# Performance work log

Hardware: AMD Instinct MI355X
Metric: run time of the kernel (lower is better)

Reference implementation:

```python
import jax, jax.numpy as jnp
import numpy as np

N_NODES = 50000


def gcn_conv(x, W, b, row, col, n):
    """PyG GCNConv with default add_self_loops=True, normalize=True.
    out[i] = sum_{e: col[e]=i} d^-1/2[row[e]] d^-1/2[i] * (x@W)[row[e]]
             + d^-1[i]*(x@W)[i] + b,  where d = in-degree + 1 (self-loop).
    """
    x_lin = x @ W                                   # [n, out_ch]
    ones = jnp.ones(row.shape[0], dtype=x.dtype)
    deg = jax.ops.segment_sum(ones, col, num_segments=n) + 1.0  # self-loop
    dinv = jax.lax.rsqrt(deg)                       # deg >= 1, safe
    norm = dinv[row] * dinv[col]                    # [E]
    msg = norm[:, None] * x_lin[row]                # [E, out_ch]
    agg = jax.ops.segment_sum(msg, col, num_segments=n)
    self_term = (dinv * dinv)[:, None] * x_lin      # self-loop contribution
    return agg + self_term + b


def setup_inputs() -> dict:
    key = jax.random.key(0)
    ks = jax.random.split(key, 10)
    in_ch, hid, out_ch = 128, 256, 64
    E = 800000
    x = jax.random.normal(ks[0], (N_NODES, in_ch), dtype=jnp.float32)
    edge_attr = jax.random.normal(ks[1], (E, 8), dtype=jnp.float32)  # unused by forward
    edge_index = jax.random.randint(ks[2], (2, E), 0, N_NODES, dtype=jnp.int64)
    def glorot(k, fan_in, fan_out):
        s = float(np.sqrt(6.0 / (fan_in + fan_out)))
        return jax.random.uniform(k, (fan_in, fan_out), jnp.float32, -s, s)
    return {
        "x": x,
        "edge_attr": edge_attr,
        "edge_index": edge_index,
        "W1": glorot(ks[3], in_ch, hid), "b1": jnp.zeros((hid,), jnp.float32),
        "W2": glorot(ks[4], hid, hid),  "b2": jnp.zeros((hid,), jnp.float32),
        "W3": glorot(ks[5], hid, out_ch), "b3": jnp.zeros((out_ch,), jnp.float32),
    }


def reference(x, edge_attr, edge_index, W1, b1, W2, b2, W3, b3):
    n = x.shape[0]
    row, col = edge_index[0], edge_index[1]
    h = jax.nn.sigmoid(gcn_conv(x, W1, b1, row, col, n))
    h = jax.nn.sigmoid(gcn_conv(h, W2, b2, row, col, n))
    # dropout(p=0.1) in eval mode is identity
    return gcn_conv(h, W3, b3, row, col, n)
```

## Files before the change

kernel.cpp:

```cpp
#include <hip/hip_runtime.h>
#include <hip/hip_bf16.h>

typedef __bf16 bf16x8_t __attribute__((ext_vector_type(8)));
typedef float f32x4_t __attribute__((ext_vector_type(4)));
typedef float f32x2_t __attribute__((ext_vector_type(2)));

__device__ __forceinline__ float bits2f(unsigned int u) {
    union { unsigned int u; float f; } c; c.u = u; return c.f;
}
__device__ __forceinline__ unsigned short f2bf_bits(float f) {
    __hip_bfloat16 h = __float2bfloat16(f);
    return __builtin_bit_cast(unsigned short, h);
}
__device__ __forceinline__ f32x2_t unpack_bf2(unsigned int u) {
    return (f32x2_t){bits2f(u << 16), bits2f(u & 0xffff0000u)};
}
__device__ __forceinline__ f32x2_t xsw(f32x2_t v, int off) {
    f32x2_t r;
    r[0] = __shfl_xor(v[0], off);
    r[1] = __shfl_xor(v[1], off);
    return r;
}

__global__ void sentinel_fill(float* __restrict__ out, int n) {
    int i = blockIdx.x * blockDim.x + threadIdx.x;
    if (i < n) out[i] = 100.0f;
}

__global__ void detect_ei(const unsigned int* __restrict__ ei, int* __restrict__ flags) {
    int lane = threadIdx.x;
    int cz = 0;
    #pragma unroll
    for (int j = 0; j < 4; ++j) {
        int idx = lane * 4 + j;
        cz += (ei[2 * idx + 1] == 0u);
    }
    #pragma unroll
    for (int off = 32; off; off >>= 1) cz += __shfl_down(cz, off);
    if (lane == 0) flags[0] = (cz > 200);
}


__global__ void count_rank_dual2(const int* __restrict__ ei, int* __restrict__ cnt,
                                 int* __restrict__ rank, int* __restrict__ c32,
                                 int* __restrict__ r32, int E, int M,
                                 const int* __restrict__ flags) {
    int e = blockIdx.x * blockDim.x + threadIdx.x;
    if (e < E) {
        int r, c;
        if (flags[0]) { r = ei[2 * e]; c = ei[2 * E + 2 * e]; }
        else          { r = ei[e];     c = ei[E + e]; }
        c32[e] = c;
        r32[e] = r;
        int rk = 0;
        if ((unsigned)c < (unsigned)M) rk = atomicAdd(&cnt[c], 1);
        rank[e] = rk;
    }
}

__global__ void scan_blocks(const int* __restrict__ cnt, int* __restrict__ excl,
                            int* __restrict__ bsum, int n) {
    int tid = threadIdx.x;
    int i = blockIdx.x * 256 + tid;
    int lane = tid & 63, wv = tid >> 6;
    __shared__ int ws[4];
    int v = (i < n) ? cnt[i] : 0;
    int s = v;
    #pragma unroll
    for (int off = 1; off < 64; off <<= 1) {
        int t = __shfl_up(s, off);
        if (lane >= off) s += t;
    }
    if (lane == 63) ws[wv] = s;
    __syncthreads();
    if (tid == 0) { int a = 0; for (int q = 0; q < 4; ++q) { int t = ws[q]; ws[q] = a; a += t; } }
    __syncthreads();
    int ex = s - v + ws[wv];
    if (i < n) excl[i] = ex;
    if (tid == 255) bsum[blockIdx.x] = ex + v;
}

__global__ void scan_bsums(const int* __restrict__ bsum, int* __restrict__ boff,
                           int nb, int* __restrict__ colptr, int n) {
    int tid = threadIdx.x, lane = tid & 63, wv = tid >> 6;
    __shared__ int ws[4];
    __shared__ int carry;
    if (tid == 0) carry = 0;
    __syncthreads();
    for (int base = 0; base < nb; base += 256) {
        int i = base + tid;
        int v = (i < nb) ? bsum[i] : 0;
        int s = v;
        #pragma unroll
        for (int off = 1; off < 64; off <<= 1) {
            int t = __shfl_up(s, off);
            if (lane >= off) s += t;
        }
        if (lane == 63) ws[wv] = s;
        __syncthreads();
        if (tid == 0) { int a = carry; for (int q = 0; q < 4; ++q) { int t = ws[q]; ws[q] = a; a += t; } carry = a; }
        __syncthreads();
        int ex = s - v + ws[wv];
        if (i < nb) boff[i] = ex;
        __syncthreads();
    }
    if (tid == 0) colptr[n] = carry;
}

__global__ void scan_add_dinv(const int* __restrict__ excl, const int* __restrict__ boff,
                              const int* __restrict__ cnt, int* __restrict__ colptr,
                              float* __restrict__ dinv, int n) {
    int i = blockIdx.x * 256 + threadIdx.x;
    if (i < n) {
        colptr[i] = excl[i] + boff[blockIdx.x];
        dinv[i] = rsqrtf((float)cnt[i] + 1.0f);
    }
}

__global__ void fill_csr_part2(const int* __restrict__ c32, const int* __restrict__ r32,
                               const int* __restrict__ colptr, const int* __restrict__ rank,
                               int* __restrict__ esrc, int E, int M, int psz) {
    int part = blockIdx.x & 7;
    int e = (blockIdx.x >> 3) * 256 + threadIdx.x;
    int lo = part * psz;
    int hi = lo + psz; if (hi > M) hi = M;
    if (e < E) {
        int c = c32[e];
        if (c >= lo && c < hi) {
            int r = r32[e];
            if ((unsigned)r < (unsigned)M) {
                int p = colptr[c] + rank[e];
                if ((unsigned)p < (unsigned)E) esrc[p] = r;
            }
        }
    }
}

__global__ void transpose_all(const float* __restrict__ W1, const float* __restrict__ W2,
                              const float* __restrict__ W3,
                              unsigned short* __restrict__ Wt1, unsigned short* __restrict__ Wt2,
                              unsigned short* __restrict__ Wt3) {
    int i = blockIdx.x * 256 + threadIdx.x;
    if (i < 32768) {
        int k = i >> 8, n = i & 255;
        Wt1[n * 128 + k] = f2bf_bits(W1[i]);
    } else if (i < 32768 + 65536) {
        int j = i - 32768;
        int k = j >> 8, n = j & 255;
        Wt2[n * 256 + k] = f2bf_bits(W2[j]);
    } else if (i < 114688) {
        int j = i - 98304;
        int k = j >> 6, n = j & 63;
        Wt3[n * 256 + k] = f2bf_bits(W3[j]);
    }
}

__global__ void prescale_x(const float* __restrict__ x, const float* __restrict__ dinv,
                           unsigned short* __restrict__ xs, int M, int total) {
    int i = blockIdx.x * 256 + threadIdx.x;
    if (i < total) {
        int row = i >> 7;
        int k = i & 127;
        xs[(size_t)(k >> 6) * ((size_t)M * 64) + (size_t)row * 64 + (k & 63)] =
            f2bf_bits(x[i] * dinv[row]);
    }
}

template<int K, int BN, int NTOT, int EPI>
__global__ __launch_bounds__(256) void gemm_tile(
    const __bf16* __restrict__ A,
    const unsigned short* __restrict__ Bt,
    const float* __restrict__ dinv,
    const float* __restrict__ bias,
    void* __restrict__ Y,
    int M)
{
    constexpr int KS = (K > 128) ? 128 : K;
    constexpr int KP = KS + 8;
    constexpr int NT = BN / 2 / 16;
    __shared__ unsigned short Bs[BN * KP];

    const int tid  = threadIdx.x;
    const int lane = tid & 63;
    const int wave = tid >> 6;
    const int wm   = wave >> 1;
    const int wn   = wave & 1;
    const int quad = lane >> 4;
    const int l16  = lane & 15;
    const int n0   = blockIdx.y * BN;

    int mrow[4];
#pragma unroll
    for (int mt = 0; mt < 4; ++mt) {
        int r = blockIdx.x * 128 + wm * 64 + mt * 16 + l16;
        mrow[mt] = (r < M) ? r : (M - 1);
    }

    f32x4_t acc[4][NT];
#pragma unroll
    for (int mt = 0; mt < 4; ++mt)
#pragma unroll
        for (int t = 0; t < NT; ++t) acc[mt][t] = (f32x4_t){0.f, 0.f, 0.f, 0.f};

    const unsigned short* BsW = &Bs[(wn * (BN / 2)) * KP];

    for (int kh = 0; kh < K; kh += KS) {
        constexpr int CH = BN * KS / 8;
        for (int idx = tid; idx < CH; idx += 256) {
            int n  = idx / (KS / 8);
            int k8 = idx - n * (KS / 8);
            uint4 v = *(const uint4*)(Bt + (size_t)(n0 + n) * K + kh + k8 * 8);
            *(uint4*)&Bs[n * KP + k8 * 8] = v;
        }
        __syncthreads();

#pragma unroll
        for (int kc = 0; kc < KS; kc += 32) {
            bf16x8_t a[4], b[NT];
#pragma unroll
            for (int mt = 0; mt < 4; ++mt)
                a[mt] = *(const bf16x8_t*)(A + (size_t)mrow[mt] * K + kh + kc + quad * 8);
#pragma unroll
            for (int t = 0; t < NT; ++t)
                b[t] = *(const bf16x8_t*)&BsW[(t * 16 + l16) * KP + kc + quad * 8];
#pragma unroll
            for (int mt = 0; mt < 4; ++mt)
#pragma unroll
                for (int t = 0; t < NT; ++t)
                    acc[mt][t] = __builtin_amdgcn_mfma_f32_16x16x32_bf16(a[mt], b[t], acc[mt][t], 0, 0, 0);
        }
        if (kh + KS < K) __syncthreads();
    }

    float bv[NT];
    if constexpr (EPI == 1) {
#pragma unroll
        for (int t = 0; t < NT; ++t)
            bv[t] = bias[n0 + wn * (BN / 2) + t * 16 + l16];
    }

#pragma unroll
    for (int mt = 0; mt < 4; ++mt) {
        int rowbase = blockIdx.x * 128 + wm * 64 + mt * 16 + quad * 4;
#pragma unroll
        for (int r = 0; r < 4; ++r) {
            int rrow = rowbase + r;
            if (rrow < M) {
                if constexpr (EPI == 0) {
                    float dv = dinv[rrow];
#pragma unroll
                    for (int t = 0; t < NT; ++t) {
                        int ccol = n0 + wn * (BN / 2) + t * 16 + l16;
                        ((__hip_bfloat16*)Y)[(size_t)rrow * NTOT + ccol] =
                            __float2bfloat16(acc[mt][t][r] * dv);
                    }
                } else if constexpr (EPI == 1) {
#pragma unroll
                    for (int t = 0; t < NT; ++t) {
                        int ccol = n0 + wn * (BN / 2) + t * 16 + l16;
                        float o = acc[mt][t][r] + bv[t];
                        o = 1.f / (1.f + __expf(-o));
                        ((__hip_bfloat16*)Y)[(size_t)rrow * NTOT + ccol] = __float2bfloat16(o);
                    }
                } else {
                    float dv = dinv[rrow];
#pragma unroll
                    for (int t = 0; t < NT; ++t) {
                        int ccol = n0 + wn * (BN / 2) + t * 16 + l16;
                        float o = acc[mt][t][r] * dv;
                        int pk = __builtin_amdgcn_cvt_pk_fp8_f32(o, o, 0, false);
                        size_t choff = (size_t)(ccol >> 7) * ((size_t)M * 128)
                                     + (size_t)rrow * 128 + (ccol & 127);
                        ((unsigned char*)Y)[choff] = (unsigned char)(pk & 0xff);
                    }
                }
            }
        }
    }
}

__global__ __launch_bounds__(256) void aggregate_fp8_c2(
    const unsigned char* __restrict__ Y8c,
    const int* __restrict__ colptr,
    const int* __restrict__ esrc,
    const float* __restrict__ dinv,
    const float* __restrict__ bias,
    unsigned short* __restrict__ H,
    int M, int Etot, int nbx)
{
    const int lane = threadIdx.x & 63;
    const int wave = threadIdx.x >> 6;
    const int sub = lane & 15;
    const int grp = lane >> 4;
    int bx = blockIdx.x;
    int chunk = (bx >= nbx) ? 1 : 0;
    if (chunk) bx -= nbx;
    int node = bx * 4 + wave;
    if (node >= M) return;

    int s = colptr[node];
    int e = colptr[node + 1];
    if (s < 0) s = 0;
    if (e > Etot) e = Etot;
    if (e < s) e = s;
    int n = e - s;

    const char* Yb = (const char*)(Y8c + (size_t)chunk * ((size_t)M * 128));
    const unsigned lb = (unsigned)(sub * 8);

    f32x2_t a0 = {0.f, 0.f}, a1 = {0.f, 0.f}, a2 = {0.f, 0.f}, a3 = {0.f, 0.f};

    if (grp == 0) {
        uint2 u = *(const uint2*)(Yb + ((unsigned)node) * 128u + lb);
        a0 += __builtin_amdgcn_cvt_pk_f32_fp8(u.x, false);
        a1 += __builtin_amdgcn_cvt_pk_f32_fp8(u.x, true);
        a2 += __builtin_amdgcn_cvt_pk_f32_fp8(u.y, false);
        a3 += __builtin_amdgcn_cvt_pk_f32_fp8(u.y, true);
    }
#pragma unroll 2
    for (int t = grp; t < n; t += 4) {
        unsigned off = ((unsigned)esrc[s + t]) * 128u + lb;
        uint2 u = *(const uint2*)(Yb + off);
        a0 += __builtin_amdgcn_cvt_pk_f32_fp8(u.x, false);
        a1 += __builtin_amdgcn_cvt_pk_f32_fp8(u.x, true);
        a2 += __builtin_amdgcn_cvt_pk_f32_fp8(u.y, false);
        a3 += __builtin_amdgcn_cvt_pk_f32_fp8(u.y, true);
    }

    a0 += xsw(a0, 16); a1 += xsw(a1, 16); a2 += xsw(a2, 16); a3 += xsw(a3, 16);
    a0 += xsw(a0, 32); a1 += xsw(a1, 32); a2 += xsw(a2, 32); a3 += xsw(a3, 32);

    if (grp == 0) {
        float dv = dinv[node];
        int chb = chunk * 128 + sub * 8;
        float4 b0 = *(const float4*)(bias + chb);
        float4 b1 = *(const float4*)(bias + chb + 4);
        float o[8];
        o[0] = a0[0] * dv + b0.x; o[1] = a0[1] * dv + b0.y;
        o[2] = a1[0] * dv + b0.z; o[3] = a1[1] * dv + b0.w;
        o[4] = a2[0] * dv + b1.x; o[5] = a2[1] * dv + b1.y;
        o[6] = a3[0] * dv + b1.z; o[7] = a3[1] * dv + b1.w;
        #pragma unroll
        for (int k = 0; k < 8; ++k) o[k] = 1.f / (1.f + __expf(-o[k]));
        uint4 st;
        st.x = (unsigned)f2bf_bits(o[0]) | ((unsigned)f2bf_bits(o[1]) << 16);
        st.y = (unsigned)f2bf_bits(o[2]) | ((unsigned)f2bf_bits(o[3]) << 16);
        st.z = (unsigned)f2bf_bits(o[4]) | ((unsigned)f2bf_bits(o[5]) << 16);
        st.w = (unsigned)f2bf_bits(o[6]) | ((unsigned)f2bf_bits(o[7]) << 16);
        *(uint4*)(H + (size_t)node * 256 + chb) = st;
    }
}

__global__ __launch_bounds__(256) void aggregate_bf16_c2(
    const unsigned short* __restrict__ Xc,
    const int* __restrict__ colptr,
    const int* __restrict__ esrc,
    const float* __restrict__ dinv,
    unsigned short* __restrict__ Hout,
    int M, int Etot, int nbx)
{
    const int lane = threadIdx.x & 63;
    const int wave = threadIdx.x >> 6;
    const int sub = lane & 15;
    const int grp = lane >> 4;
    int bx = blockIdx.x;
    int chunk = (bx >= nbx) ? 1 : 0;
    if (chunk) bx -= nbx;
    int node = bx * 4 + wave;
    if (node >= M) return;

    int s = colptr[node];
    int e = colptr[node + 1];
    if (s < 0) s = 0;
    if (e > Etot) e = Etot;
    if (e < s) e = s;
    int n = e - s;

    const char* Yb = (const char*)(Xc + (size_t)chunk * ((size_t)M * 64));
    const unsigned lb = (unsigned)(sub * 8);

    f32x2_t a0 = {0.f, 0.f}, a1 = {0.f, 0.f};

    if (grp == 0) {
        uint2 u = *(const uint2*)(Yb + ((unsigned)node) * 128u + lb);
        a0 += unpack_bf2(u.x);
        a1 += unpack_bf2(u.y);
    }
#pragma unroll 2
    for (int t = grp; t < n; t += 4) {
        unsigned off = ((unsigned)esrc[s + t]) * 128u + lb;
        uint2 u = *(const uint2*)(Yb + off);
        a0 += unpack_bf2(u.x);
        a1 += unpack_bf2(u.y);
    }

    a0 += xsw(a0, 16); a1 += xsw(a1, 16);
    a0 += xsw(a0, 32); a1 += xsw(a1, 32);

    if (grp == 0) {
        float dv = dinv[node];
        uint2 st;
        st.x = (unsigned)f2bf_bits(a0[0] * dv) | ((unsigned)f2bf_bits(a0[1] * dv) << 16);
        st.y = (unsigned)f2bf_bits(a1[0] * dv) | ((unsigned)f2bf_bits(a1[1] * dv) << 16);
        *(uint2*)(Hout + (size_t)node * 128 + chunk * 64 + sub * 4) = st;
    }
}

__global__ __launch_bounds__(256) void aggregate_bf16_64_v3(
    const unsigned short* __restrict__ Yin,
    const int* __restrict__ colptr,
    const int* __restrict__ esrc,
    const float* __restrict__ dinv,
    const float* __restrict__ bias,
    float* __restrict__ out,
    int M, int Etot)
{
    const int lane = threadIdx.x & 63;
    const int wave = threadIdx.x >> 6;
    const int sub = lane & 15;
    const int grp = lane >> 4;
    int node = blockIdx.x * 4 + wave;
    if (node >= M) return;

    int s = colptr[node];
    int e = colptr[node + 1];
    if (s < 0) s = 0;
    if (e > Etot) e = Etot;
    if (e < s) e = s;
    int n = e - s;

    const char* Yb = (const char*)Yin;
    const unsigned lb = (unsigned)(sub * 8);

    f32x2_t a0 = {0.f, 0.f}, a1 = {0.f, 0.f};

    if (grp == 0) {
        uint2 u = *(const uint2*)(Yb + ((unsigned)node) * 128u + lb);
        a0 += unpack_bf2(u.x);
        a1 += unpack_bf2(u.y);
    }
#pragma unroll 2
    for (int t = grp; t < n; t += 4) {
        unsigned off = ((unsigned)esrc[s + t]) * 128u + lb;
        uint2 u = *(const uint2*)(Yb + off);
        a0 += unpack_bf2(u.x);
        a1 += unpack_bf2(u.y);
    }

    a0 += xsw(a0, 16); a1 += xsw(a1, 16);
    a0 += xsw(a0, 32); a1 += xsw(a1, 32);

    if (grp == 0) {
        float dv = dinv[node];
        float4 bv = *(const float4*)(bias + sub * 4);
        float4 st;
        st.x = a0[0] * dv + bv.x;
        st.y = a0[1] * dv + bv.y;
        st.z = a1[0] * dv + bv.z;
        st.w = a1[1] * dv + bv.w;
        *(float4*)(out + (size_t)node * 64 + sub * 4) = st;
    }
}


extern "C" void kernel_launch(void* const* d_in, const int* in_sizes, int n_in,
                              void* d_out, int out_size, void* d_ws, size_t ws_size,
                              hipStream_t stream)
{
    int iEI = 2, iW1 = 3, iB1 = 4, iW2 = 5, iB2 = 6, iW3 = 7, iB3 = 8;
    if (n_in == 8) { iEI = 1; iW1 = 2; iB1 = 3; iW2 = 4; iB2 = 5; iW3 = 6; iB3 = 7; }

    const float* x  = (const float*)d_in[0];
    const int* ei   = (const int*)d_in[iEI];
    const float* W1 = (const float*)d_in[iW1];
    const float* b1 = (const float*)d_in[iB1];
    const float* W2 = (const float*)d_in[iW2];
    const float* b2 = (const float*)d_in[iB2];
    const float* W3 = (const float*)d_in[iW3];
    const float* b3 = (const float*)d_in[iB3];

    const int M = in_sizes[0] / 128;
    const int E = in_sizes[iEI] / 2;
    const int NB = (M + 255) / 256;
    const int PSZ = (M + 7) / 8;

    auto rnd = [](size_t b) { return (b + 255) & ~(size_t)255; };
    size_t needed = rnd(64 * 4)
                  + rnd((size_t)M * 4) * 2
                  + rnd((size_t)(M + 1) * 4)
                  + rnd((size_t)M * 4)
                  + rnd((size_t)(NB + 1) * 4) * 2
                  + rnd((size_t)E * 4) * 4
                  + rnd((size_t)256 * 128 * 2)
                  + rnd((size_t)256 * 256 * 2)
                  + rnd((size_t)64 * 256 * 2)
                  + rnd((size_t)M * 256 * 2) * 2;
    if (ws_size < needed) {
        sentinel_fill<<<(out_size + 255) / 256, 256, 0, stream>>>((float*)d_out, out_size);
        return;
    }

    char* p = (char*)d_ws;
    auto alloc = [&](size_t bytes) {
        char* r = p;
        p += (bytes + 255) & ~(size_t)255;
        return r;
    };
    int* flags  = (int*)alloc(64 * 4);
    float* dinv = (float*)alloc((size_t)M * 4);
    int* cnt    = (int*)alloc((size_t)M * 4);
    int* colptr = (int*)alloc((size_t)(M + 1) * 4);
    int* excl   = (int*)alloc((size_t)M * 4);
    int* bsum   = (int*)alloc((size_t)(NB + 1) * 4);
    int* boff   = (int*)alloc((size_t)(NB + 1) * 4);
    int* esrc   = (int*)alloc((size_t)E * 4);
    int* rank   = (int*)alloc((size_t)E * 4);
    int* c32    = (int*)alloc((size_t)E * 4);
    int* r32    = (int*)alloc((size_t)E * 4);
    unsigned short* Wt1 = (unsigned short*)alloc((size_t)256 * 128 * 2);
    unsigned short* Wt2 = (unsigned short*)alloc((size_t)256 * 256 * 2);
    unsigned short* Wt3 = (unsigned short*)alloc((size_t)64 * 256 * 2);
    __hip_bfloat16* ybuf = (__hip_bfloat16*)alloc((size_t)M * 256 * 2);
    __hip_bfloat16* hbuf = (__hip_bfloat16*)alloc((size_t)M * 256 * 2);

    unsigned short* xs = (unsigned short*)ybuf;
    unsigned short* xa = (unsigned short*)ybuf + (size_t)M * 128;
    unsigned char*  y8 = (unsigned char*)ybuf;

    detect_ei<<<1, 64, 0, stream>>>((const unsigned int*)ei, flags);

    hipMemsetAsync(cnt, 0, (size_t)M * 4, stream);
    count_rank_dual2<<<(E + 255) / 256, 256, 0, stream>>>(ei, cnt, rank, c32, r32, E, M, flags);
    scan_blocks<<<NB, 256, 0, stream>>>(cnt, excl, bsum, M);
    scan_bsums<<<1, 256, 0, stream>>>(bsum, boff, NB, colptr, M);
    scan_add_dinv<<<NB, 256, 0, stream>>>(excl, boff, cnt, colptr, dinv, M);
    fill_csr_part2<<<((E + 255) / 256) * 8, 256, 0, stream>>>(
        c32, r32, colptr, rank, esrc, E, M, PSZ);
    transpose_all<<<(114688 + 255) / 256, 256, 0, stream>>>(W1, W2, W3, Wt1, Wt2, Wt3);

    int gmb = (M + 127) / 128;
    int ga  = (M + 3) / 4;

    prescale_x<<<((M * 128) + 255) / 256, 256, 0, stream>>>(x, dinv, xs, M, M * 128);
    aggregate_bf16_c2<<<2 * ga, 256, 0, stream>>>(
        xs, colptr, esrc, dinv, xa, M, E, ga);
    gemm_tile<128, 128, 256, 1><<<dim3(gmb, 2), 256, 0, stream>>>(
        (const __bf16*)xa, Wt1, dinv, b1, hbuf, M);
    gemm_tile<256, 128, 256, 2><<<dim3(gmb, 2), 256, 0, stream>>>(
        (const __bf16*)hbuf, Wt2, dinv, b2, y8, M);
    aggregate_fp8_c2<<<2 * ga, 256, 0, stream>>>(
        y8, colptr, esrc, dinv, b2, (unsigned short*)hbuf, M, E, ga);
    gemm_tile<256, 64, 64, 0><<<dim3(gmb, 1), 256, 0, stream>>>(
        (const __bf16*)hbuf, Wt3, dinv, b3, ybuf, M);
    aggregate_bf16_64_v3<<<ga, 256, 0, stream>>>(
        (const unsigned short*)ybuf, colptr, esrc, dinv, b3, (float*)d_out, M, E);
}
```

Before: 369.8 us.

## Quantize prescaled input to fp8, fuse prep kernels, software-pipeline gathers

Prescaled x is now stored as fp8 with 128 channels per row in a single chunk rather than two bf16 chunks, so the first aggregation moves half the bytes and runs in one pass. The weight transpose is folded into the same prep launch. All three aggregation kernels now double-buffer their gathers, loading the next 8 edges before accumulating the current ones. The layer-2 fp8 aggregation interleaves its two channel chunks across neighbouring blocks for better locality. Quantizing the input to fp8 loses precision in the first layer.

```diff
diff --git a/kernel.cpp b/kernel.cpp
--- a/kernel.cpp
+++ b/kernel.cpp
@@ -14,12 +14,6 @@
 }
 __device__ __forceinline__ f32x2_t unpack_bf2(unsigned int u) {
     return (f32x2_t){bits2f(u << 16), bits2f(u & 0xffff0000u)};
-}
-__device__ __forceinline__ f32x2_t xsw(f32x2_t v, int off) {
-    f32x2_t r;
-    r[0] = __shfl_xor(v[0], off);
-    r[1] = __shfl_xor(v[1], off);
-    return r;
 }
 
 __global__ void sentinel_fill(float* __restrict__ out, int n) {
@@ -136,33 +130,37 @@
     }
 }
 
-__global__ void transpose_all(const float* __restrict__ W1, const float* __restrict__ W2,
-                              const float* __restrict__ W3,
-                              unsigned short* __restrict__ Wt1, unsigned short* __restrict__ Wt2,
-                              unsigned short* __restrict__ Wt3) {
-    int i = blockIdx.x * 256 + threadIdx.x;
-    if (i < 32768) {
-        int k = i >> 8, n = i & 255;
-        Wt1[n * 128 + k] = f2bf_bits(W1[i]);
-    } else if (i < 32768 + 65536) {
-        int j = i - 32768;
-        int k = j >> 8, n = j & 255;
-        Wt2[n * 256 + k] = f2bf_bits(W2[j]);
-    } else if (i < 114688) {
-        int j = i - 98304;
-        int k = j >> 6, n = j & 63;
-        Wt3[n * 256 + k] = f2bf_bits(W3[j]);
-    }
-}
-
-__global__ void prescale_x(const float* __restrict__ x, const float* __restrict__ dinv,
-                           unsigned short* __restrict__ xs, int M, int total) {
-    int i = blockIdx.x * 256 + threadIdx.x;
-    if (i < total) {
-        int row = i >> 7;
-        int k = i & 127;
-        xs[(size_t)(k >> 6) * ((size_t)M * 64) + (size_t)row * 64 + (k & 63)] =
-            f2bf_bits(x[i] * dinv[row]);
+__global__ void prep_fused(const float* __restrict__ x, const float* __restrict__ dinv,
+                           unsigned char* __restrict__ xs8,
+                           const float* __restrict__ W1, const float* __restrict__ W2,
+                           const float* __restrict__ W3,
+                           unsigned short* __restrict__ Wt1, unsigned short* __restrict__ Wt2,
+                           unsigned short* __restrict__ Wt3,
+                           int M, int nps) {
+    if ((int)blockIdx.x < nps) {
+        int i = blockIdx.x * 256 + threadIdx.x;
+        if (i < M * 32) {
+            int row = i >> 5;
+            float dv = dinv[row];
+            float4 v = *(const float4*)(x + (size_t)i * 4);
+            unsigned u = __builtin_amdgcn_cvt_pk_fp8_f32(v.x * dv, v.y * dv, 0, false);
+            u = __builtin_amdgcn_cvt_pk_fp8_f32(v.z * dv, v.w * dv, u, true);
+            *(unsigned*)(xs8 + (size_t)i * 4) = u;
+        }
+    } else {
+        int i = ((int)blockIdx.x - nps) * 256 + threadIdx.x;
+        if (i < 32768) {
+            int k = i >> 8, n = i & 255;
+            Wt1[n * 128 + k] = f2bf_bits(W1[i]);
+        } else if (i < 32768 + 65536) {
+            int j = i - 32768;
+            int k = j >> 8, n = j & 255;
+            Wt2[n * 256 + k] = f2bf_bits(W2[j]);
+        } else if (i < 114688) {
+            int j = i - 98304;
+            int k = j >> 6, n = j & 63;
+            Wt3[n * 256 + k] = f2bf_bits(W3[j]);
+        }
     }
 }
 
@@ -279,23 +277,25 @@
     }
 }
 
-__global__ __launch_bounds__(256) void aggregate_fp8_c2(
+__global__ __launch_bounds__(256) void aggregate_fp8_x2b(
     const unsigned char* __restrict__ Y8c,
     const int* __restrict__ colptr,
     const int* __restrict__ esrc,
     const float* __restrict__ dinv,
     const float* __restrict__ bias,
     unsigned short* __restrict__ H,
-    int M, int Etot, int nbx)
+    int M, int Etot, int ga)
 {
     const int lane = threadIdx.x & 63;
     const int wave = threadIdx.x >> 6;
-    const int sub = lane & 15;
-    const int grp = lane >> 4;
-    int bx = blockIdx.x;
-    int chunk = (bx >= nbx) ? 1 : 0;
-    if (chunk) bx -= nbx;
-    int node = bx * 4 + wave;
+    const int l4 = lane & 15;
+    const int g4 = lane >> 4;
+
+    int s8 = blockIdx.x & 7;
+    int chunk = s8 >> 2;
+    int grp = (blockIdx.x >> 3) * 4 + (s8 & 3);
+    if (grp >= ga) return;
+    int node = grp * 4 + wave;
     if (node >= M) return;
 
     int s = colptr[node];
@@ -306,33 +306,66 @@
     int n = e - s;
 
     const char* Yb = (const char*)(Y8c + (size_t)chunk * ((size_t)M * 128));
-    const unsigned lb = (unsigned)(sub * 8);
+    const unsigned lb = (unsigned)(l4 * 8);
+
+    uint2 su = {0u, 0u};
+    if (g4 == 0) su = *(const uint2*)(Yb + ((unsigned)node) * 128u + lb);
 
     f32x2_t a0 = {0.f, 0.f}, a1 = {0.f, 0.f}, a2 = {0.f, 0.f}, a3 = {0.f, 0.f};
 
-    if (grp == 0) {
-        uint2 u = *(const uint2*)(Yb + ((unsigned)node) * 128u + lb);
-        a0 += __builtin_amdgcn_cvt_pk_f32_fp8(u.x, false);
-        a1 += __builtin_amdgcn_cvt_pk_f32_fp8(u.x, true);
-        a2 += __builtin_amdgcn_cvt_pk_f32_fp8(u.y, false);
-        a3 += __builtin_amdgcn_cvt_pk_f32_fp8(u.y, true);
-    }
-#pragma unroll 2
-    for (int t = grp; t < n; t += 4) {
-        unsigned off = ((unsigned)esrc[s + t]) * 128u + lb;
-        uint2 u = *(const uint2*)(Yb + off);
-        a0 += __builtin_amdgcn_cvt_pk_f32_fp8(u.x, false);
-        a1 += __builtin_amdgcn_cvt_pk_f32_fp8(u.x, true);
-        a2 += __builtin_amdgcn_cvt_pk_f32_fp8(u.y, false);
-        a3 += __builtin_amdgcn_cvt_pk_f32_fp8(u.y, true);
-    }
-
-    a0 += xsw(a0, 16); a1 += xsw(a1, 16); a2 += xsw(a2, 16); a3 += xsw(a3, 16);
-    a0 += xsw(a0, 32); a1 += xsw(a1, 32); a2 += xsw(a2, 32); a3 += xsw(a3, 32);
-
-    if (grp == 0) {
+    auto gat = [&](uint2* u, int base) {
+        u[0] = *(const uint2*)(Yb + ((unsigned)esrc[s + base + g4]) * 128u + lb);
+        u[1] = *(const uint2*)(Yb + ((unsigned)esrc[s + base + 4 + g4]) * 128u + lb);
+    };
+    auto acc = [&](const uint2* u) {
+        #pragma unroll
+        for (int k = 0; k < 2; ++k) {
+            a0 += __builtin_amdgcn_cvt_pk_f32_fp8(u[k].x, false);
+            a1 += __builtin_amdgcn_cvt_pk_f32_fp8(u[k].x, true);
+            a2 += __builtin_amdgcn_cvt_pk_f32_fp8(u[k].y, false);
+            a3 += __builtin_amdgcn_cvt_pk_f32_fp8(u[k].y, true);
+        }
+    };
+
+    uint2 ua[2], ub[2];
+    int NB = n >> 3;
+    if (NB > 0) {
+        gat(ua, 0);
+        int i = 1;
+        for (; i + 1 < NB; i += 2) {
+            gat(ub, i << 3); acc(ua);
+            gat(ua, (i + 1) << 3); acc(ub);
+        }
+        if (i < NB) { gat(ub, i << 3); acc(ua); acc(ub); }
+        else acc(ua);
+    }
+    for (int t = NB << 3; t < n; t += 4) {
+        if (t + g4 < n) {
+            uint2 u = *(const uint2*)(Yb + ((unsigned)esrc[s + t + g4]) * 128u + lb);
+            a0 += __builtin_amdgcn_cvt_pk_f32_fp8(u.x, false);
+            a1 += __builtin_amdgcn_cvt_pk_f32_fp8(u.x, true);
+            a2 += __builtin_amdgcn_cvt_pk_f32_fp8(u.y, false);
+            a3 += __builtin_amdgcn_cvt_pk_f32_fp8(u.y, true);
+        }
+    }
+    if (g4 == 0) {
+        a0 += __builtin_amdgcn_cvt_pk_f32_fp8(su.x, false);
+        a1 += __builtin_amdgcn_cvt_pk_f32_fp8(su.x, true);
+        a2 += __builtin_amdgcn_cvt_pk_f32_fp8(su.y, false);
+        a3 += __builtin_amdgcn_cvt_pk_f32_fp8(su.y, true);
+    }
+
+    #pragma unroll
+    for (int off = 16; off < 64; off <<= 1) {
+        a0[0] += __shfl_xor(a0[0], off); a0[1] += __shfl_xor(a0[1], off);
+        a1[0] += __shfl_xor(a1[0], off); a1[1] += __shfl_xor(a1[1], off);
+        a2[0] += __shfl_xor(a2[0], off); a2[1] += __shfl_xor(a2[1], off);
+        a3[0] += __shfl_xor(a3[0], off); a3[1] += __shfl_xor(a3[1], off);
+    }
+
+    if (g4 == 0) {
         float dv = dinv[node];
-        int chb = chunk * 128 + sub * 8;
+        int chb = chunk * 128 + l4 * 8;
         float4 b0 = *(const float4*)(bias + chb);
         float4 b1 = *(const float4*)(bias + chb + 4);
         float o[8];
@@ -351,22 +384,19 @@
     }
 }
 
-__global__ __launch_bounds__(256) void aggregate_bf16_c2(
-    const unsigned short* __restrict__ Xc,
+__global__ __launch_bounds__(256) void aggregate_xs8b(
+    const unsigned char* __restrict__ X8,
     const int* __restrict__ colptr,
     const int* __restrict__ esrc,
     const float* __restrict__ dinv,
-    unsigned short* __restrict__ Hout,
-    int M, int Etot, int nbx)
+    unsigned short* __restrict__ xa,
+    int M, int Etot)
 {
     const int lane = threadIdx.x & 63;
     const int wave = threadIdx.x >> 6;
-    const int sub = lane & 15;
-    const int grp = lane >> 4;
-    int bx = blockIdx.x;
-    int chunk = (bx >= nbx) ? 1 : 0;
-    if (chunk) bx -= nbx;
-    int node = bx * 4 + wave;
+    const int l4 = lane & 15;
+    const int g4 = lane >> 4;
+    int node = blockIdx.x * 4 + wave;
     if (node >= M) return;
 
     int s = colptr[node];
@@ -376,37 +406,76 @@
     if (e < s) e = s;
     int n = e - s;
 
-    const char* Yb = (const char*)(Xc + (size_t)chunk * ((size_t)M * 64));
-    const unsigned lb = (unsigned)(sub * 8);
-
-    f32x2_t a0 = {0.f, 0.f}, a1 = {0.f, 0.f};
-
-    if (grp == 0) {
-        uint2 u = *(const uint2*)(Yb + ((unsigned)node) * 128u + lb);
-        a0 += unpack_bf2(u.x);
-        a1 += unpack_bf2(u.y);
-    }
-#pragma unroll 2
-    for (int t = grp; t < n; t += 4) {
-        unsigned off = ((unsigned)esrc[s + t]) * 128u + lb;
-        uint2 u = *(const uint2*)(Yb + off);
-        a0 += unpack_bf2(u.x);
-        a1 += unpack_bf2(u.y);
-    }
-
-    a0 += xsw(a0, 16); a1 += xsw(a1, 16);
-    a0 += xsw(a0, 32); a1 += xsw(a1, 32);
-
-    if (grp == 0) {
+    const char* Yb = (const char*)X8;
+    const unsigned lb = (unsigned)(l4 * 8);
+
+    uint2 su = {0u, 0u};
+    if (g4 == 0) su = *(const uint2*)(Yb + ((unsigned)node) * 128u + lb);
+
+    f32x2_t a0 = {0.f, 0.f}, a1 = {0.f, 0.f}, a2 = {0.f, 0.f}, a3 = {0.f, 0.f};
+
+    auto gat = [&](uint2* u, int base) {
+        u[0] = *(const uint2*)(Yb + ((unsigned)esrc[s + base + g4]) * 128u + lb);
+        u[1] = *(const uint2*)(Yb + ((unsigned)esrc[s + base + 4 + g4]) * 128u + lb);
+    };
+    auto acc = [&](const uint2* u) {
+        #pragma unroll
+        for (int k = 0; k < 2; ++k) {
+            a0 += __builtin_amdgcn_cvt_pk_f32_fp8(u[k].x, false);
+            a1 += __builtin_amdgcn_cvt_pk_f32_fp8(u[k].x, true);
+            a2 += __builtin_amdgcn_cvt_pk_f32_fp8(u[k].y, false);
+            a3 += __builtin_amdgcn_cvt_pk_f32_fp8(u[k].y, true);
+        }
+    };
+
+    uint2 ua[2], ub[2];
+    int NB = n >> 3;
+    if (NB > 0) {
+        gat(ua, 0);
+        int i = 1;
+        for (; i + 1 < NB; i += 2) {
+            gat(ub, i << 3); acc(ua);
+            gat(ua, (i + 1) << 3); acc(ub);
+        }
+        if (i < NB) { gat(ub, i << 3); acc(ua); acc(ub); }
+        else acc(ua);
+    }
+    for (int t = NB << 3; t < n; t += 4) {
+        if (t + g4 < n) {
+            uint2 u = *(const uint2*)(Yb + ((unsigned)esrc[s + t + g4]) * 128u + lb);
+            a0 += __builtin_amdgcn_cvt_pk_f32_fp8(u.x, false);
+            a1 += __builtin_amdgcn_cvt_pk_f32_fp8(u.x, true);
+            a2 += __builtin_amdgcn_cvt_pk_f32_fp8(u.y, false);
+            a3 += __builtin_amdgcn_cvt_pk_f32_fp8(u.y, true);
+        }
+    }
+    if (g4 == 0) {
+        a0 += __builtin_amdgcn_cvt_pk_f32_fp8(su.x, false);
+        a1 += __builtin_amdgcn_cvt_pk_f32_fp8(su.x, true);
+        a2 += __builtin_amdgcn_cvt_pk_f32_fp8(su.y, false);
+        a3 += __builtin_amdgcn_cvt_pk_f32_fp8(su.y, true);
+    }
+
+    #pragma unroll
+    for (int off = 16; off < 64; off <<= 1) {
+        a0[0] += __shfl_xor(a0[0], off); a0[1] += __shfl_xor(a0[1], off);
+        a1[0] += __shfl_xor(a1[0], off); a1[1] += __shfl_xor(a1[1], off);
+        a2[0] += __shfl_xor(a2[0], off); a2[1] += __shfl_xor(a2[1], off);
+        a3[0] += __shfl_xor(a3[0], off); a3[1] += __shfl_xor(a3[1], off);
+    }
+
+    if (g4 == 0) {
         float dv = dinv[node];
-        uint2 st;
+        uint4 st;
         st.x = (unsigned)f2bf_bits(a0[0] * dv) | ((unsigned)f2bf_bits(a0[1] * dv) << 16);
         st.y = (unsigned)f2bf_bits(a1[0] * dv) | ((unsigned)f2bf_bits(a1[1] * dv) << 16);
-        *(uint2*)(Hout + (size_t)node * 128 + chunk * 64 + sub * 4) = st;
-    }
-}
-
-__global__ __launch_bounds__(256) void aggregate_bf16_64_v3(
+        st.z = (unsigned)f2bf_bits(a2[0] * dv) | ((unsigned)f2bf_bits(a2[1] * dv) << 16);
+        st.w = (unsigned)f2bf_bits(a3[0] * dv) | ((unsigned)f2bf_bits(a3[1] * dv) << 16);
+        *(uint4*)(xa + (size_t)node * 128 + l4 * 8) = st;
+    }
+}
+
+__global__ __launch_bounds__(256) void aggregate_bf16_64_v5(
     const unsigned short* __restrict__ Yin,
     const int* __restrict__ colptr,
     const int* __restrict__ esrc,
@@ -417,8 +486,8 @@
 {
     const int lane = threadIdx.x & 63;
     const int wave = threadIdx.x >> 6;
-    const int sub = lane & 15;
-    const int grp = lane >> 4;
+    const int l4 = lane & 15;
+    const int g4 = lane >> 4;
     int node = blockIdx.x * 4 + wave;
     if (node >= M) return;
 
@@ -430,35 +499,64 @@
     int n = e - s;
 
     const char* Yb = (const char*)Yin;
-    const unsigned lb = (unsigned)(sub * 8);
+    const unsigned lb = (unsigned)(l4 * 8);
+
+    uint2 su = {0u, 0u};
+    if (g4 == 0) su = *(const uint2*)(Yb + ((unsigned)node) * 128u + lb);
 
     f32x2_t a0 = {0.f, 0.f}, a1 = {0.f, 0.f};
 
-    if (grp == 0) {
-        uint2 u = *(const uint2*)(Yb + ((unsigned)node) * 128u + lb);
-        a0 += unpack_bf2(u.x);
-        a1 += unpack_bf2(u.y);
-    }
-#pragma unroll 2
-    for (int t = grp; t < n; t += 4) {
-        unsigned off = ((unsigned)esrc[s + t]) * 128u + lb;
-        uint2 u = *(const uint2*)(Yb + off);
-        a0 += unpack_bf2(u.x);
-        a1 += unpack_bf2(u.y);
-    }
-
-    a0 += xsw(a0, 16); a1 += xsw(a1, 16);
-    a0 += xsw(a0, 32); a1 += xsw(a1, 32);
-
-    if (grp == 0) {
+    auto gat = [&](uint2* u, int base) {
+        u[0] = *(const uint2*)(Yb + ((unsigned)esrc[s + base + g4]) * 128u + lb);
+        u[1] = *(const uint2*)(Yb + ((unsigned)esrc[s + base + 4 + g4]) * 128u + lb);
+    };
+    auto acc = [&](const uint2* u) {
+        #pragma unroll
+        for (int k = 0; k < 2; ++k) {
+            a0 += unpack_bf2(u[k].x);
+            a1 += unpack_bf2(u[k].y);
+        }
+    };
+
+    uint2 ua[2], ub[2];
+    int NB = n >> 3;
+    if (NB > 0) {
+        gat(ua, 0);
+        int i = 1;
+        for (; i + 1 < NB; i += 2) {
+            gat(ub, i << 3); acc(ua);
+            gat(ua, (i + 1) << 3); acc(ub);
+        }
+        if (i < NB) { gat(ub, i << 3); acc(ua); acc(ub); }
+        else acc(ua);
+    }
+    for (int t = NB << 3; t < n; t += 4) {
+        if (t + g4 < n) {
+            uint2 u = *(const uint2*)(Yb + ((unsigned)esrc[s + t + g4]) * 128u + lb);
+            a0 += unpack_bf2(u.x);
+            a1 += unpack_bf2(u.y);
+        }
+    }
+    if (g4 == 0) {
+        a0 += unpack_bf2(su.x);
+        a1 += unpack_bf2(su.y);
+    }
+
+    #pragma unroll
+    for (int off = 16; off < 64; off <<= 1) {
+        a0[0] += __shfl_xor(a0[0], off); a0[1] += __shfl_xor(a0[1], off);
+        a1[0] += __shfl_xor(a1[0], off); a1[1] += __shfl_xor(a1[1], off);
+    }
+
+    if (g4 == 0) {
         float dv = dinv[node];
-        float4 bv = *(const float4*)(bias + sub * 4);
+        float4 bv = *(const float4*)(bias + l4 * 4);
         float4 st;
         st.x = a0[0] * dv + bv.x;
         st.y = a0[1] * dv + bv.y;
         st.z = a1[0] * dv + bv.z;
         st.w = a1[1] * dv + bv.w;
-        *(float4*)(out + (size_t)node * 64 + sub * 4) = st;
+        *(float4*)(out + (size_t)node * 64 + l4 * 4) = st;
     }
 }
 
@@ -523,7 +621,7 @@
     __hip_bfloat16* ybuf = (__hip_bfloat16*)alloc((size_t)M * 256 * 2);
     __hip_bfloat16* hbuf = (__hip_bfloat16*)alloc((size_t)M * 256 * 2);
 
-    unsigned short* xs = (unsigned short*)ybuf;
+    unsigned char* xs8 = (unsigned char*)ybuf;
     unsigned short* xa = (unsigned short*)ybuf + (size_t)M * 128;
     unsigned char*  y8 = (unsigned char*)ybuf;
 
@@ -536,22 +634,25 @@
     scan_add_dinv<<<NB, 256, 0, stream>>>(excl, boff, cnt, colptr, dinv, M);
     fill_csr_part2<<<((E + 255) / 256) * 8, 256, 0, stream>>>(
         c32, r32, colptr, rank, esrc, E, M, PSZ);
-    transpose_all<<<(114688 + 255) / 256, 256, 0, stream>>>(W1, W2, W3, Wt1, Wt2, Wt3);
 
     int gmb = (M + 127) / 128;
     int ga  = (M + 3) / 4;
-
-    prescale_x<<<((M * 128) + 255) / 256, 256, 0, stream>>>(x, dinv, xs, M, M * 128);
-    aggregate_bf16_c2<<<2 * ga, 256, 0, stream>>>(
-        xs, colptr, esrc, dinv, xa, M, E, ga);
+    int nps = (M * 32 + 255) / 256;
+    int nsup = (ga + 3) / 4;
+
+    prep_fused<<<nps + 448, 256, 0, stream>>>(
+        x, dinv, xs8, W1, W2, W3, Wt1, Wt2, Wt3, M, nps);
+
+    aggregate_xs8b<<<ga, 256, 0, stream>>>(
+        xs8, colptr, esrc, dinv, xa, M, E);
     gemm_tile<128, 128, 256, 1><<<dim3(gmb, 2), 256, 0, stream>>>(
         (const __bf16*)xa, Wt1, dinv, b1, hbuf, M);
     gemm_tile<256, 128, 256, 2><<<dim3(gmb, 2), 256, 0, stream>>>(
         (const __bf16*)hbuf, Wt2, dinv, b2, y8, M);
-    aggregate_fp8_c2<<<2 * ga, 256, 0, stream>>>(
+    aggregate_fp8_x2b<<<nsup * 8, 256, 0, stream>>>(
         y8, colptr, esrc, dinv, b2, (unsigned short*)hbuf, M, E, ga);
     gemm_tile<256, 64, 64, 0><<<dim3(gmb, 1), 256, 0, stream>>>(
         (const __bf16*)hbuf, Wt3, dinv, b3, ybuf, M);
-    aggregate_bf16_64_v3<<<ga, 256, 0, stream>>>(
+    aggregate_bf16_64_v5<<<ga, 256, 0, stream>>>(
         (const unsigned short*)ybuf, colptr, esrc, dinv, b3, (float*)d_out, M, E);
 }
```

Measured after the change: 344.6 us. -6.8%, faster.
